# Performance work log

Measured on AMD Instinct MI355X. Metric: run time of the kernel, lower is better.

The kernel has to match this reference:

```python
import jax, jax.numpy as jnp
import numpy as np

B, T, D, V = 32, 2048, 256, 2048  # batch, time, embed_dim, num_codebooks


def setup_inputs() -> dict:
    key = jax.random.key(0)
    k1, k2 = jax.random.split(key)
    z = jax.random.normal(k1, (B, T, D), dtype=jnp.float32)
    codebook_weight = jax.random.normal(k2, (V, D), dtype=jnp.float32)
    return {"z": z, "codebook_weight": codebook_weight}


def reference(z, codebook_weight):
    # e = codebook.embedding.weight.clone().detach()
    e = jax.lax.stop_gradient(codebook_weight)            # (V, D)
    zf = z.reshape(-1, e.shape[1])                        # (N, D), N = B*T
    # squared euclidean distances via GEMM expansion
    d = (jnp.sum(zf * zf, axis=1, keepdims=True)
         + jnp.sum(e * e, axis=1)
         - 2.0 * zf @ e.T)                                # (N, V)
    idx = jnp.argmin(d, axis=1)                           # (N,)
    # one-hot matmul with e is mathematically a row gather of e
    z_q = jnp.take(e, idx, axis=0).reshape(z.shape)       # (B, T, D)
    commitment_loss = jnp.mean((z - jax.lax.stop_gradient(z_q)) ** 2)
    z_q_st = z + jax.lax.stop_gradient(z_q - z)           # straight-through
    encoding_indices = idx.reshape(z.shape[0], z.shape[1])  # (B, T)
    hist = jnp.bincount(idx, length=V).astype(jnp.float32)
    codebook_prob = hist / (hist.sum() + 1e-8)
    return commitment_loss, z_q_st, encoding_indices, codebook_prob
```

## Files before the change

### kernel.cpp

```cpp
#include <hip/hip_runtime.h>

#define NROWS 65536
#define DIM   256
#define VCB   2048
#define DELTA 0.25f

typedef _Float16 f16;
typedef _Float16 f16x8 __attribute__((ext_vector_type(8)));
typedef float    f32x4 __attribute__((ext_vector_type(4)));


__device__ __forceinline__ void async16(void* lds, const void* g) {
  __builtin_amdgcn_global_load_lds(
      (const __attribute__((address_space(1))) void*)g,
      (__attribute__((address_space(3))) void*)lds, 16, 0, 0);
}

__global__ __launch_bounds__(256) void convert_kernel(
    const float4* __restrict__ src, short4* __restrict__ dhi,
    short4* __restrict__ dlo, int n4) {
  int stride = gridDim.x * 256;
  for (int i = blockIdx.x * 256 + threadIdx.x; i < n4; i += stride) {
    float4 v = src[i];
    union { f16 h[4]; short4 s; } H, L;
    H.h[0] = (f16)v.x; H.h[1] = (f16)v.y; H.h[2] = (f16)v.z; H.h[3] = (f16)v.w;
    L.h[0] = (f16)(v.x - (float)H.h[0]);
    L.h[1] = (f16)(v.y - (float)H.h[1]);
    L.h[2] = (f16)(v.z - (float)H.h[2]);
    L.h[3] = (f16)(v.w - (float)H.h[3]);
    dhi[i] = H.s; dlo[i] = L.s;
  }
}

__global__ __launch_bounds__(256) void prep_kernel(
    const float* __restrict__ e, float* __restrict__ enorm,
    unsigned int* __restrict__ hist, double* __restrict__ loss_part,
    int* __restrict__ flag_cnt) {
  int tid = threadIdx.x;
  int gt = blockIdx.x * 256 + tid;
  if (gt == 0) flag_cnt[0] = 0;
  if (gt < VCB) hist[gt] = 0u;
  if (gt < 256) loss_part[gt] = 0.0;
  int wid  = gt >> 6;
  int lane = tid & 63;
  if (wid < VCB) {
    const float4* row = (const float4*)(e + (size_t)wid * DIM);
    float4 v = row[lane];
    float s = v.x*v.x + v.y*v.y + v.z*v.z + v.w*v.w;
    #pragma unroll
    for (int off = 32; off; off >>= 1) s += __shfl_xor(s, off);
    if (lane == 0) enorm[wid] = s;
  }
}

__global__ __launch_bounds__(512) void pass1_kernel(
    const float* __restrict__ z, const f16* __restrict__ eh,
    const float* __restrict__ enorm,
    int* __restrict__ idx_out, unsigned int* __restrict__ hist,
    double* __restrict__ loss_part,
    int* __restrict__ flag_cnt, int* __restrict__ flag_list) {
  __shared__ f16 ldsA[8][4096];
  __shared__ f16 ldsB[3][8192];
  __shared__ float sx1[3][2][64];
  __shared__ float sx2[3][2][64];
  __shared__ int   sxi[3][2][64];

  const int tid  = threadIdx.x;
  const int wid  = tid >> 6;
  const int lane = tid & 63;
  const int wr   = wid >> 2;
  const int wc   = wid & 3;
  const int lrow = lane & 15;
  const int lq   = lane >> 4;
  const int rbase = blockIdx.x * 128;

  auto stageB = [&](int b, int ss, int kt) {
    #pragma unroll
    for (int i = 0; i < 2; ++i) {
      int col   = wid * 32 + i * 16 + (lane >> 2);
      int chunk = lane & 3;
      int gk    = chunk ^ ((col >> 1) & 3);
      size_t goff = (size_t)(ss * 256 + col) * DIM + (kt << 5) + (gk << 3);
      async16(&ldsB[b][0] + col * 32 + chunk * 8, eh + goff);
    }
  };

  {
    const int row = tid >> 2;
    const int q   = tid & 3;
    const float* zrow = z + (size_t)(rbase + row) * DIM + q * 64;
    const int sw = (row >> 1) & 3;
    float zs = 0.f;
    #pragma unroll
    for (int f = 0; f < 16; ++f) {
      float4 v = *(const float4*)(zrow + f * 4);
      int col4   = q * 64 + f * 4;
      int kt     = col4 >> 5;
      int ko     = col4 & 31;
      int chunk  = ko >> 3;
      int within = (ko & 7) * 2;
      int addr = kt * 8192 + row * 64 + ((chunk ^ sw) << 4) + within;
      union { f16 h[4]; short4 s4; } H;
      H.h[0] = (f16)v.x; H.h[1] = (f16)v.y; H.h[2] = (f16)v.z; H.h[3] = (f16)v.w;
      *(short4*)((char*)ldsA + addr) = H.s4;
      zs += v.x*v.x + v.y*v.y + v.z*v.z + v.w*v.w;
    }
    #pragma unroll
    for (int off = 32; off; off >>= 1) zs += __shfl_xor(zs, off);
    if (lane == 0) atomicAdd(&loss_part[blockIdx.x & 255], (double)zs);
  }
  stageB(0, 0, 0);
  asm volatile("s_waitcnt vmcnt(0)" ::: "memory");
  __syncthreads();

  float m1[4][4], m2v[4][4];
  int   i1[4][4];
  #pragma unroll
  for (int m = 0; m < 4; ++m)
    #pragma unroll
    for (int r = 0; r < 4; ++r) { m1[m][r] = 3.4e38f; m2v[m][r] = 3.4e38f; i1[m][r] = 0; }

  const int cchunk = lq ^ ((lrow >> 1) & 3);

  int pb = 0;
  for (int ss = 0; ss < 8; ++ss) {
    f32x4 acc[4][4];
    #pragma unroll
    for (int m = 0; m < 4; ++m)
      #pragma unroll
      for (int n = 0; n < 4; ++n) {
        f32x4 zz = {0.f, 0.f, 0.f, 0.f};
        acc[m][n] = zz;
      }

    for (int kt = 0; kt < 8; ++kt) {
      int nkt = kt + 1, nss = ss;
      if (nkt == 8) { nkt = 0; ++nss; if (nss == 8) nss = 0; }
      int nxt = pb + 1; if (nxt == 3) nxt = 0;
      stageB(nxt, nss, nkt);
      asm volatile("s_waitcnt vmcnt(2)" ::: "memory");
      asm volatile("s_barrier" ::: "memory");
      __builtin_amdgcn_sched_barrier(0);

      const char* abase = (const char*)&ldsA[kt][0];
      f16x8 ah[4];
      #pragma unroll
      for (int m = 0; m < 4; ++m) {
        int row = wr * 64 + m * 16 + lrow;
        ah[m] = *(const f16x8*)(abase + row * 64 + cchunk * 16);
      }
      const char* bbase = (const char*)&ldsB[pb][0];
      #pragma unroll
      for (int n = 0; n < 4; ++n) {
        int col = wc * 64 + n * 16 + lrow;
        f16x8 bh = *(const f16x8*)(bbase + col * 64 + cchunk * 16);
        #pragma unroll
        for (int m = 0; m < 4; ++m)
          acc[m][n] = __builtin_amdgcn_mfma_f32_16x16x32_f16(ah[m], bh, acc[m][n], 0, 0, 0);
      }
      pb = nxt;
    }

    #pragma unroll
    for (int n = 0; n < 4; ++n) {
      int j = ss * 256 + wc * 64 + n * 16 + lrow;
      float en = enorm[j];
      #pragma unroll
      for (int m = 0; m < 4; ++m)
        #pragma unroll
        for (int r = 0; r < 4; ++r) {
          float s = fmaf(-2.f, acc[m][n][r], en);
          if (s < m1[m][r]) { m2v[m][r] = m1[m][r]; m1[m][r] = s; i1[m][r] = j; }
          else if (s < m2v[m][r]) m2v[m][r] = s;
        }
    }
  }
  asm volatile("s_waitcnt vmcnt(0)" ::: "memory");

  #pragma unroll
  for (int off = 1; off < 16; off <<= 1) {
    #pragma unroll
    for (int m = 0; m < 4; ++m)
      #pragma unroll
      for (int r = 0; r < 4; ++r) {
        float o1 = __shfl_xor(m1[m][r], off);
        int   oi = __shfl_xor(i1[m][r], off);
        float o2 = __shfl_xor(m2v[m][r], off);
        float nm2 = fminf(fminf(m2v[m][r], o2), fmaxf(m1[m][r], o1));
        if (o1 < m1[m][r] || (o1 == m1[m][r] && oi < i1[m][r])) {
          m1[m][r] = o1; i1[m][r] = oi;
        }
        m2v[m][r] = nm2;
      }
  }

  __syncthreads();
  if (wc != 0 && lrow == 0) {
    #pragma unroll
    for (int m = 0; m < 4; ++m)
      #pragma unroll
      for (int r = 0; r < 4; ++r) {
        int li = m * 16 + lq * 4 + r;
        sx1[wc - 1][wr][li] = m1[m][r];
        sx2[wc - 1][wr][li] = m2v[m][r];
        sxi[wc - 1][wr][li] = i1[m][r];
      }
  }
  __syncthreads();
  if (wc == 0 && lrow == 0) {
    float lsum = 0.f;
    #pragma unroll
    for (int m = 0; m < 4; ++m)
      #pragma unroll
      for (int r = 0; r < 4; ++r) {
        int li = m * 16 + lq * 4 + r;
        float v  = m1[m][r];
        int   bi = i1[m][r];
        float v2 = m2v[m][r];
        #pragma unroll
        for (int g = 0; g < 3; ++g) {
          float ov = sx1[g][wr][li];
          float o2 = sx2[g][wr][li];
          int   oi = sxi[g][wr][li];
          float nm2 = fminf(fminf(v2, o2), fmaxf(v, ov));
          if (ov < v || (ov == v && oi < bi)) { v = ov; bi = oi; }
          v2 = nm2;
        }
        int row = rbase + wr * 64 + li;
        if (v2 - v <= DELTA) {
          int p = atomicAdd(flag_cnt, 1);
          flag_list[p] = row;
        } else {
          idx_out[row] = bi;
          atomicAdd(&hist[bi], 1u);
          lsum += v;
        }
      }
    lsum += __shfl_xor(lsum, 16);
    lsum += __shfl_xor(lsum, 32);
    if (lane == 0) atomicAdd(&loss_part[blockIdx.x & 255], (double)lsum);
  }
}

__global__ __launch_bounds__(512) void pass2_kernel(
    const float* __restrict__ z,
    const f16* __restrict__ eh, const f16* __restrict__ el,
    const float* __restrict__ enorm,
    const int* __restrict__ flag_cnt, const int* __restrict__ flag_list,
    float* __restrict__ pval, int* __restrict__ pidx) {
  __shared__ f16 ldsA[8][8192];
  __shared__ f16 ldsB[2][8192];

  const int tid  = threadIdx.x;
  const int wid  = tid >> 6;
  const int lane = tid & 63;
  const int wr   = wid >> 2;
  const int wc   = wid & 3;
  const int lrow = lane & 15;
  const int lq   = lane >> 4;
  const int srow = tid >> 2;
  const int scol = tid & 3;
  const int skoff = ((scol ^ ((srow >> 1) & 3)) << 3);
  const int cchunk = lq ^ ((lrow >> 1) & 3);
  const int cnt = *flag_cnt;

  auto stageB = [&](int b, int vcol, int kt) {
    size_t off = (size_t)(vcol + srow) * DIM + (kt << 5) + skoff;
    async16(&ldsB[b][0]    + tid * 8, eh + off);
    async16(&ldsB[b][4096] + tid * 8, el + off);
  };

  for (int job = blockIdx.x; ; job += gridDim.x) {
    int chunk = job >> 4, cb = job & 15;
    int base = chunk * 128;
    if (base >= cnt) break;
    int nrows = cnt - base; if (nrows > 128) nrows = 128;

    __syncthreads();

    {
      const int row = tid >> 2;
      const int q   = tid & 3;
      int grow = flag_list[base + (row < nrows ? row : 0)];
      const float* zrow = z + (size_t)grow * DIM + q * 64;
      const int sw = (row >> 1) & 3;
      #pragma unroll
      for (int f = 0; f < 16; ++f) {
        float4 v = *(const float4*)(zrow + f * 4);
        int col4   = q * 64 + f * 4;
        int kt     = col4 >> 5;
        int ko     = col4 & 31;
        int chunk2 = ko >> 3;
        int within = (ko & 7) * 2;
        int addr = kt * 16384 + row * 64 + ((chunk2 ^ sw) << 4) + within;
        union { f16 h[4]; short4 s4; } H, L;
        H.h[0] = (f16)v.x; H.h[1] = (f16)v.y; H.h[2] = (f16)v.z; H.h[3] = (f16)v.w;
        L.h[0] = (f16)(v.x - (float)H.h[0]);
        L.h[1] = (f16)(v.y - (float)H.h[1]);
        L.h[2] = (f16)(v.z - (float)H.h[2]);
        L.h[3] = (f16)(v.w - (float)H.h[3]);
        *(short4*)((char*)ldsA + addr)        = H.s4;
        *(short4*)((char*)ldsA + addr + 8192) = L.s4;
      }
    }
    int pb = 0;
    stageB(0, cb * 128, 0);
    asm volatile("s_waitcnt vmcnt(0)" ::: "memory");
    __syncthreads();

    float minv[4][4];
    int   mini[4][4];
    #pragma unroll
    for (int m = 0; m < 4; ++m)
      #pragma unroll
      for (int r = 0; r < 4; ++r) { minv[m][r] = 3.4e38f; mini[m][r] = 0; }

    f32x4 acc[4][2];
    #pragma unroll
    for (int m = 0; m < 4; ++m)
      #pragma unroll
      for (int n = 0; n < 2; ++n) {
        f32x4 zz = {0.f, 0.f, 0.f, 0.f};
        acc[m][n] = zz;
      }

    for (int kt = 0; kt < 8; ++kt) {
      if (kt < 7) {
        stageB(pb ^ 1, cb * 128, kt + 1);
        asm volatile("s_waitcnt vmcnt(2)" ::: "memory");
      } else {
        asm volatile("s_waitcnt vmcnt(0)" ::: "memory");
      }
      asm volatile("s_barrier" ::: "memory");
      __builtin_amdgcn_sched_barrier(0);

      const char* abase = (const char*)&ldsA[kt][0];
      f16x8 ah[4], al[4];
      #pragma unroll
      for (int m = 0; m < 4; ++m) {
        int row = wr * 64 + m * 16 + lrow;
        int off = row * 64 + cchunk * 16;
        ah[m] = *(const f16x8*)(abase + off);
        al[m] = *(const f16x8*)(abase + 8192 + off);
      }
      const char* bbase = (const char*)&ldsB[pb][0];
      #pragma unroll
      for (int n = 0; n < 2; ++n) {
        int col = wc * 32 + n * 16 + lrow;
        int off = col * 64 + cchunk * 16;
        f16x8 bh = *(const f16x8*)(bbase + off);
        f16x8 bl = *(const f16x8*)(bbase + 8192 + off);
        #pragma unroll
        for (int m = 0; m < 4; ++m) {
          acc[m][n] = __builtin_amdgcn_mfma_f32_16x16x32_f16(ah[m], bh, acc[m][n], 0, 0, 0);
          acc[m][n] = __builtin_amdgcn_mfma_f32_16x16x32_f16(ah[m], bl, acc[m][n], 0, 0, 0);
          acc[m][n] = __builtin_amdgcn_mfma_f32_16x16x32_f16(al[m], bh, acc[m][n], 0, 0, 0);
        }
      }
      __builtin_amdgcn_sched_barrier(0);
      asm volatile("s_barrier" ::: "memory");
      pb ^= 1;
    }

    #pragma unroll
    for (int n = 0; n < 2; ++n) {
      int j = cb * 128 + wc * 32 + n * 16 + lrow;
      float en = enorm[j];
      #pragma unroll
      for (int m = 0; m < 4; ++m)
        #pragma unroll
        for (int r = 0; r < 4; ++r) {
          float s = fmaf(-2.f, acc[m][n][r], en);
          if (s < minv[m][r]) { minv[m][r] = s; mini[m][r] = j; }
        }
    }

    #pragma unroll
    for (int off = 1; off < 16; off <<= 1) {
      #pragma unroll
      for (int m = 0; m < 4; ++m)
        #pragma unroll
        for (int r = 0; r < 4; ++r) {
          float ov = __shfl_xor(minv[m][r], off);
          int   oi = __shfl_xor(mini[m][r], off);
          if (ov < minv[m][r] || (ov == minv[m][r] && oi < mini[m][r])) {
            minv[m][r] = ov; mini[m][r] = oi;
          }
        }
    }

    __syncthreads();
    float* sxv = (float*)&ldsB[0][0];
    int*   sxi2 = (int*)(sxv + 3 * 2 * 64);
    if (wc != 0 && lrow == 0) {
      #pragma unroll
      for (int m = 0; m < 4; ++m)
        #pragma unroll
        for (int r = 0; r < 4; ++r) {
          int li = m * 16 + lq * 4 + r;
          int ix = ((wc - 1) * 2 + wr) * 64 + li;
          sxv[ix] = minv[m][r];
          sxi2[ix] = mini[m][r];
        }
    }
    __syncthreads();
    if (wc == 0 && lrow == 0) {
      #pragma unroll
      for (int m = 0; m < 4; ++m)
        #pragma unroll
        for (int r = 0; r < 4; ++r) {
          int li = m * 16 + lq * 4 + r;
          float v  = minv[m][r];
          int   bi = mini[m][r];
          #pragma unroll
          for (int g = 0; g < 3; ++g) {
            int ix = (g * 2 + wr) * 64 + li;
            float ov = sxv[ix];
            int   oi = sxi2[ix];
            if (ov < v || (ov == v && oi < bi)) { v = ov; bi = oi; }
          }
          int i = wr * 64 + li;
          if (i < nrows) {
            int fi = base + i;
            pval[fi * 16 + cb] = v;
            pidx[fi * 16 + cb] = bi;
          }
        }
    }
  }
}

__global__ __launch_bounds__(256) void pass2m_kernel(
    const int* __restrict__ flag_cnt, const int* __restrict__ flag_list,
    const float* __restrict__ pval, const int* __restrict__ pidx,
    int* __restrict__ idx_out, unsigned int* __restrict__ hist,
    double* __restrict__ loss_part) {
  int cnt = *flag_cnt;
  int t = blockIdx.x * 256 + threadIdx.x;
  int stride = gridDim.x * 256;
  for (int fi = t; fi < cnt; fi += stride) {
    float m = 3.4e38f; int bi = 0;
    #pragma unroll
    for (int cb = 0; cb < 16; ++cb) {
      float v = pval[fi * 16 + cb];
      int  ix = pidx[fi * 16 + cb];
      if (v < m || (v == m && ix < bi)) { m = v; bi = ix; }
    }
    int row = flag_list[fi];
    idx_out[row] = bi;
    atomicAdd(&hist[bi], 1u);
    atomicAdd(&loss_part[fi & 255], (double)m);
  }
}

__global__ __launch_bounds__(256) void gather_kernel(
    const float* __restrict__ e, const int* __restrict__ idx,
    float* __restrict__ zq_out, float* __restrict__ idxf_out) {
  int tid  = threadIdx.x;
  int w    = tid >> 6;
  int lane = tid & 63;
  int n    = blockIdx.x * 4 + w;

  int ci = idx[n];
  const float4* er = (const float4*)(e + (size_t)ci * DIM);
  ((float4*)(zq_out + (size_t)n * DIM))[lane] = er[lane];
  if (lane == 0) idxf_out[n] = (float)ci;
}

__global__ __launch_bounds__(256) void finalize_kernel(
    const unsigned int* __restrict__ hist, const double* __restrict__ loss_part,
    float* __restrict__ out) {
  __shared__ double lsh[4];
  __shared__ float  hsh[4];
  __shared__ float  denom_sh;
  int tid = threadIdx.x, lane = tid & 63, w = tid >> 6;

  float hs = 0.f;
  for (int j = tid; j < VCB; j += 256) hs += (float)hist[j];
  double ls = loss_part[tid];
  #pragma unroll
  for (int off = 32; off; off >>= 1) {
    hs += __shfl_xor(hs, off);
    ls += __shfl_xor(ls, off);
  }
  if (lane == 0) { lsh[w] = ls; hsh[w] = hs; }
  __syncthreads();
  if (tid == 0) {
    double lt = lsh[0] + lsh[1] + lsh[2] + lsh[3];
    float  ht = hsh[0] + hsh[1] + hsh[2] + hsh[3];
    out[0] = (float)(lt / (double)((size_t)NROWS * DIM));
    denom_sh = ht + 1e-8f;
  }
  __syncthreads();
  float denom = denom_sh;
  float* prob = out + 1 + (size_t)NROWS * DIM + NROWS;
  for (int j = tid; j < VCB; j += 256) prob[j] = (float)hist[j] / denom;
}

extern "C" void kernel_launch(void* const* d_in, const int* in_sizes, int n_in,
                              void* d_out, int out_size, void* d_ws, size_t ws_size,
                              hipStream_t stream) {
  (void)in_sizes; (void)n_in; (void)out_size; (void)ws_size;
  const float* z = (const float*)d_in[0];
  const float* e = (const float*)d_in[1];
  float* out = (float*)d_out;
  char*  ws  = (char*)d_ws;

  int*          idx       = (int*)ws;
  unsigned int* hist      = (unsigned int*)(ws + 262144);
  double*       loss_part = (double*)(ws + 270336);
  float*        enorm     = (float*)(ws + 272384);
  int*          flag_cnt  = (int*)(ws + 280576);
  f16*          e_hi      = (f16*)(ws + 524288);
  f16*          e_lo      = (f16*)(ws + 1572864);

  float* pval      = out + 32;
  int*   pidx      = (int*)(out + 32 + 1048576);
  int*   flag_list = (int*)(out + 32 + 2097152);

  float* out_zq  = out + 1;
  float* out_idx = out + 1 + (size_t)NROWS * DIM;

  convert_kernel<<<128, 256, 0, stream>>>(
      (const float4*)e, (short4*)e_hi, (short4*)e_lo, VCB * DIM / 4);
  prep_kernel<<<512, 256, 0, stream>>>(e, enorm, hist, loss_part, flag_cnt);
  pass1_kernel<<<NROWS / 128, 512, 0, stream>>>(
      z, e_hi, enorm, idx, hist, loss_part, flag_cnt, flag_list);
  pass2_kernel<<<512, 512, 0, stream>>>(
      z, e_hi, e_lo, enorm, flag_cnt, flag_list, pval, pidx);
  pass2m_kernel<<<64, 256, 0, stream>>>(
      flag_cnt, flag_list, pval, pidx, idx, hist, loss_part);
  gather_kernel<<<NROWS / 4, 256, 0, stream>>>(e, idx, out_zq, out_idx);
  finalize_kernel<<<1, 256, 0, stream>>>(hist, loss_part, out);
}
```

Before: 212.6 us.

## Halve pass1 row tile to 64 rows and reuse B buffer for reduction scratch

Pass1 now processes 64 rows per block instead of 128. This halves the A tile in LDS and the per-wave accumulator and min-tracking registers, and doubles the grid. The cross-wave reduction scratch arrays now alias the B staging buffer instead of being separate shared arrays, which cuts LDS use further. The aim is higher occupancy and more blocks in flight. The cost is that every codebook B tile is loaded and staged twice as often per row, lowering arithmetic intensity of the MFMA loop.

```diff
diff --git a/kernel.cpp b/kernel.cpp
--- a/kernel.cpp
+++ b/kernel.cpp
@@ -59,11 +59,8 @@
     int* __restrict__ idx_out, unsigned int* __restrict__ hist,
     double* __restrict__ loss_part,
     int* __restrict__ flag_cnt, int* __restrict__ flag_list) {
-  __shared__ f16 ldsA[8][4096];
+  __shared__ f16 ldsA[8][2048];
   __shared__ f16 ldsB[3][8192];
-  __shared__ float sx1[3][2][64];
-  __shared__ float sx2[3][2][64];
-  __shared__ int   sxi[3][2][64];
 
   const int tid  = threadIdx.x;
   const int wid  = tid >> 6;
@@ -72,7 +69,7 @@
   const int wc   = wid & 3;
   const int lrow = lane & 15;
   const int lq   = lane >> 4;
-  const int rbase = blockIdx.x * 128;
+  const int rbase = blockIdx.x * 64;
 
   auto stageB = [&](int b, int ss, int kt) {
     #pragma unroll
@@ -86,20 +83,17 @@
   };
 
   {
-    const int row = tid >> 2;
-    const int q   = tid & 3;
-    const float* zrow = z + (size_t)(rbase + row) * DIM + q * 64;
+    const int row = tid >> 3;
+    const int q   = tid & 7;
+    const float* zrow = z + (size_t)(rbase + row) * DIM + q * 32;
     const int sw = (row >> 1) & 3;
     float zs = 0.f;
     #pragma unroll
-    for (int f = 0; f < 16; ++f) {
+    for (int f = 0; f < 8; ++f) {
       float4 v = *(const float4*)(zrow + f * 4);
-      int col4   = q * 64 + f * 4;
-      int kt     = col4 >> 5;
-      int ko     = col4 & 31;
-      int chunk  = ko >> 3;
-      int within = (ko & 7) * 2;
-      int addr = kt * 8192 + row * 64 + ((chunk ^ sw) << 4) + within;
+      int chunk  = f >> 1;
+      int within = (f & 1) * 8;
+      int addr = q * 4096 + row * 64 + ((chunk ^ sw) << 4) + within;
       union { f16 h[4]; short4 s4; } H;
       H.h[0] = (f16)v.x; H.h[1] = (f16)v.y; H.h[2] = (f16)v.z; H.h[3] = (f16)v.w;
       *(short4*)((char*)ldsA + addr) = H.s4;
@@ -113,10 +107,10 @@
   asm volatile("s_waitcnt vmcnt(0)" ::: "memory");
   __syncthreads();
 
-  float m1[4][4], m2v[4][4];
-  int   i1[4][4];
+  float m1[2][4], m2v[2][4];
+  int   i1[2][4];
   #pragma unroll
-  for (int m = 0; m < 4; ++m)
+  for (int m = 0; m < 2; ++m)
     #pragma unroll
     for (int r = 0; r < 4; ++r) { m1[m][r] = 3.4e38f; m2v[m][r] = 3.4e38f; i1[m][r] = 0; }
 
@@ -124,9 +118,9 @@
 
   int pb = 0;
   for (int ss = 0; ss < 8; ++ss) {
-    f32x4 acc[4][4];
-    #pragma unroll
-    for (int m = 0; m < 4; ++m)
+    f32x4 acc[2][4];
+    #pragma unroll
+    for (int m = 0; m < 2; ++m)
       #pragma unroll
       for (int n = 0; n < 4; ++n) {
         f32x4 zz = {0.f, 0.f, 0.f, 0.f};
@@ -142,11 +136,11 @@
       asm volatile("s_barrier" ::: "memory");
       __builtin_amdgcn_sched_barrier(0);
 
-      const char* abase = (const char*)&ldsA[kt][0];
-      f16x8 ah[4];
-      #pragma unroll
-      for (int m = 0; m < 4; ++m) {
-        int row = wr * 64 + m * 16 + lrow;
+      const char* abase = (const char*)ldsA + kt * 4096;
+      f16x8 ah[2];
+      #pragma unroll
+      for (int m = 0; m < 2; ++m) {
+        int row = wr * 32 + m * 16 + lrow;
         ah[m] = *(const f16x8*)(abase + row * 64 + cchunk * 16);
       }
       const char* bbase = (const char*)&ldsB[pb][0];
@@ -155,7 +149,7 @@
         int col = wc * 64 + n * 16 + lrow;
         f16x8 bh = *(const f16x8*)(bbase + col * 64 + cchunk * 16);
         #pragma unroll
-        for (int m = 0; m < 4; ++m)
+        for (int m = 0; m < 2; ++m)
           acc[m][n] = __builtin_amdgcn_mfma_f32_16x16x32_f16(ah[m], bh, acc[m][n], 0, 0, 0);
       }
       pb = nxt;
@@ -166,7 +160,7 @@
       int j = ss * 256 + wc * 64 + n * 16 + lrow;
       float en = enorm[j];
       #pragma unroll
-      for (int m = 0; m < 4; ++m)
+      for (int m = 0; m < 2; ++m)
         #pragma unroll
         for (int r = 0; r < 4; ++r) {
           float s = fmaf(-2.f, acc[m][n][r], en);
@@ -180,7 +174,7 @@
   #pragma unroll
   for (int off = 1; off < 16; off <<= 1) {
     #pragma unroll
-    for (int m = 0; m < 4; ++m)
+    for (int m = 0; m < 2; ++m)
       #pragma unroll
       for (int r = 0; r < 4; ++r) {
         float o1 = __shfl_xor(m1[m][r], off);
@@ -195,22 +189,26 @@
   }
 
   __syncthreads();
+  float* sx1 = (float*)&ldsB[0][0];
+  float* sx2 = sx1 + 3 * 2 * 32;
+  int*   sxi = (int*)(sx2 + 3 * 2 * 32);
   if (wc != 0 && lrow == 0) {
     #pragma unroll
-    for (int m = 0; m < 4; ++m)
+    for (int m = 0; m < 2; ++m)
       #pragma unroll
       for (int r = 0; r < 4; ++r) {
         int li = m * 16 + lq * 4 + r;
-        sx1[wc - 1][wr][li] = m1[m][r];
-        sx2[wc - 1][wr][li] = m2v[m][r];
-        sxi[wc - 1][wr][li] = i1[m][r];
+        int ix = ((wc - 1) * 2 + wr) * 32 + li;
+        sx1[ix] = m1[m][r];
+        sx2[ix] = m2v[m][r];
+        sxi[ix] = i1[m][r];
       }
   }
   __syncthreads();
   if (wc == 0 && lrow == 0) {
     float lsum = 0.f;
     #pragma unroll
-    for (int m = 0; m < 4; ++m)
+    for (int m = 0; m < 2; ++m)
       #pragma unroll
       for (int r = 0; r < 4; ++r) {
         int li = m * 16 + lq * 4 + r;
@@ -219,14 +217,15 @@
         float v2 = m2v[m][r];
         #pragma unroll
         for (int g = 0; g < 3; ++g) {
-          float ov = sx1[g][wr][li];
-          float o2 = sx2[g][wr][li];
-          int   oi = sxi[g][wr][li];
+          int ix = (g * 2 + wr) * 32 + li;
+          float ov = sx1[ix];
+          float o2 = sx2[ix];
+          int   oi = sxi[ix];
           float nm2 = fminf(fminf(v2, o2), fmaxf(v, ov));
           if (ov < v || (ov == v && oi < bi)) { v = ov; bi = oi; }
           v2 = nm2;
         }
-        int row = rbase + wr * 64 + li;
+        int row = rbase + wr * 32 + li;
         if (v2 - v <= DELTA) {
           int p = atomicAdd(flag_cnt, 1);
           flag_list[p] = row;
@@ -524,7 +523,7 @@
   convert_kernel<<<128, 256, 0, stream>>>(
       (const float4*)e, (short4*)e_hi, (short4*)e_lo, VCB * DIM / 4);
   prep_kernel<<<512, 256, 0, stream>>>(e, enorm, hist, loss_part, flag_cnt);
-  pass1_kernel<<<NROWS / 128, 512, 0, stream>>>(
+  pass1_kernel<<<NROWS / 64, 512, 0, stream>>>(
       z, e_hi, enorm, idx, hist, loss_part, flag_cnt, flag_list);
   pass2_kernel<<<512, 512, 0, stream>>>(
       z, e_hi, e_lo, enorm, flag_cnt, flag_list, pval, pidx);
```

Result: no change. 211.3 us (-0.6%).
